# Optimization experiments

Measured on AMD Instinct MI355X. Metric: run time of the kernel, lower is better.

## Reference

```python
import jax, jax.numpy as jnp
import numpy as np
from jax import ops

NEG_SLOPE = 0.2
EPS = 1e-5


def layer_norm(v, g, b):
    mu = jnp.mean(v, axis=-1, keepdims=True)
    var = jnp.mean(jnp.square(v - mu), axis=-1, keepdims=True)
    return (v - mu) * jax.lax.rsqrt(var + EPS) * g + b


def gat_conv(x, src, dst, W, a_src, a_dst, bias, N, H, C, concat):
    # linear projection, per-head view [N, H, C]
    h = (x @ W).reshape(N, H, C)
    alpha_src = jnp.sum(h * a_src, axis=-1)  # [N, H]
    alpha_dst = jnp.sum(h * a_dst, axis=-1)  # [N, H]
    # per-edge raw attention logits [E, H]
    e = alpha_src[src] + alpha_dst[dst]
    e = jnp.where(e > 0, e, NEG_SLOPE * e)  # leaky relu
    # segment softmax over destination node
    m = ops.segment_max(e, dst, num_segments=N)  # [N, H]
    a = jnp.exp(e - m[dst])
    s = ops.segment_sum(a, dst, num_segments=N)  # [N, H]
    a = a / s[dst]
    # weighted scatter-aggregate: [E, H, C] messages -> [N, H, C]
    out = ops.segment_sum(h[src] * a[:, :, None], dst, num_segments=N)
    if concat:
        return out.reshape(N, H * C) + bias
    return jnp.mean(out, axis=1) + bias


def setup_inputs() -> dict:
    key = jax.random.key(0)
    ks = jax.random.split(key, 16)
    N, E, IN, H, C1, C2 = 50000, 800000, 128, 4, 64, 64
    sd_in = 1.0 / np.sqrt(IN)
    sd_h = 1.0 / np.sqrt(H * C1)
    return {
        "x": jax.random.normal(ks[0], (N, IN), jnp.float32),
        "edge_index": jax.random.randint(ks[1], (2, E), 0, N, jnp.int64),
        # GAT layer 1 (in -> H*C1, concat)
        "W1": jax.random.normal(ks[2], (IN, H * C1), jnp.float32) * sd_in,
        "att_src1": jax.random.normal(ks[3], (H, C1), jnp.float32) * sd_in,
        "att_dst1": jax.random.normal(ks[4], (H, C1), jnp.float32) * sd_in,
        "bias1": jnp.zeros((H * C1,), jnp.float32),
        "g1": jnp.ones((H * C1,), jnp.float32),
        "b1": jnp.zeros((H * C1,), jnp.float32),
        # GAT layer 2 (H*C1 -> C2, mean over heads)
        "W2": jax.random.normal(ks[5], (H * C1, H * C2), jnp.float32) * sd_h,
        "att_src2": jax.random.normal(ks[6], (H, C2), jnp.float32) * sd_h,
        "att_dst2": jax.random.normal(ks[7], (H, C2), jnp.float32) * sd_h,
        "bias2": jnp.zeros((C2,), jnp.float32),
        "g2": jnp.ones((C2,), jnp.float32),
        "b2": jnp.zeros((C2,), jnp.float32),
        # residual projection (in != out)
        "Wres": jax.random.normal(ks[8], (IN, C2), jnp.float32) * sd_in,
        "bres": jnp.zeros((C2,), jnp.float32),
    }


def reference(x, edge_index, W1, att_src1, att_dst1, bias1, g1, b1,
              W2, att_src2, att_dst2, bias2, g2, b2, Wres, bres):
    N = x.shape[0]
    H, C1 = att_src1.shape
    C2 = att_src2.shape[1]
    # PyG GATConv add_self_loops=True
    loop = jnp.arange(N, dtype=edge_index.dtype)
    src = jnp.concatenate([edge_index[0], loop])
    dst = jnp.concatenate([edge_index[1], loop])

    identity = x @ Wres + bres
    h1 = gat_conv(x, src, dst, W1, att_src1, att_dst1, bias1, N, H, C1, concat=True)
    h1 = jax.nn.elu(layer_norm(h1, g1, b1))  # dropout inactive (eval)
    h2 = gat_conv(h1, src, dst, W2, att_src2, att_dst2, bias2, N, H, C2, concat=False)
    h2 = layer_norm(h2, g2, b2)
    return jax.nn.elu(h2 + identity)
```

## Files before the change

### kernel.cpp

```cpp
#include <hip/hip_runtime.h>
#include <math.h>

#define HH 4
#define CC 64
#define HC 256
#define CAP 96

static constexpr float NEG_SLOPE = 0.2f;
static constexpr float LN_EPS = 1e-5f;

typedef __attribute__((ext_vector_type(8))) short short8;
typedef __attribute__((ext_vector_type(4))) float floatx4;
typedef __attribute__((ext_vector_type(4))) unsigned int uintx4;

__device__ __forceinline__ float bf2f(unsigned short u) {
  return __uint_as_float(((unsigned int)u) << 16);
}
__device__ __forceinline__ unsigned short f2bf(float f) {
  unsigned int u = __float_as_uint(f);
  u = (u + 0x7fff + ((u >> 16) & 1)) >> 16;
  return (unsigned short)u;
}
__device__ __forceinline__ unsigned int pack2bf(float a, float b) {
  return (unsigned int)f2bf(a) | ((unsigned int)f2bf(b) << 16);
}

__device__ __forceinline__ void macc8(float* acc, uintx4 h, float w) {
  acc[0] += w * __uint_as_float(h.x << 16);
  acc[1] += w * __uint_as_float(h.x & 0xffff0000u);
  acc[2] += w * __uint_as_float(h.y << 16);
  acc[3] += w * __uint_as_float(h.y & 0xffff0000u);
  acc[4] += w * __uint_as_float(h.z << 16);
  acc[5] += w * __uint_as_float(h.z & 0xffff0000u);
  acc[6] += w * __uint_as_float(h.w << 16);
  acc[7] += w * __uint_as_float(h.w & 0xffff0000u);
}

__device__ __forceinline__ short8 ldA8(const unsigned short* A, size_t idx) {
  return *(const short8*)(A + idx);
}
__device__ __forceinline__ short8 ldA8(const float* A, size_t idx) {
  const float4 u = *(const float4*)(A + idx);
  const float4 v = *(const float4*)(A + idx + 4);
  short8 r;
  r[0] = (short)f2bf(u.x); r[1] = (short)f2bf(u.y);
  r[2] = (short)f2bf(u.z); r[3] = (short)f2bf(u.w);
  r[4] = (short)f2bf(v.x); r[5] = (short)f2bf(v.y);
  r[6] = (short)f2bf(v.z); r[7] = (short)f2bf(v.w);
  return r;
}

__global__ __launch_bounds__(256) void prep_kernel(
    const float* __restrict__ W1, const float* __restrict__ W2,
    const float* __restrict__ Wres,
    unsigned short* __restrict__ wt1c, unsigned short* __restrict__ wt2,
    int* __restrict__ deg, int N) {
  const int idx = blockIdx.x * 256 + threadIdx.x;
  if (idx < 49152) {
    const int r = idx >> 7, k = idx & 127;
    float v = 0.f;
    if (r < 256) v = W1[k * 256 + r];
    else if (r < 320) v = Wres[k * 64 + (r - 256)];
    wt1c[idx] = f2bf(v);
  } else if (idx < 49152 + 65536) {
    const int i = idx - 49152;
    const int r = i >> 8, k = i & 255;
    wt2[i] = f2bf(W2[k * 256 + r]);
  } else if (idx < 49152 + 65536 + N) {
    deg[idx - 49152 - 65536] = 0;
  }
}

template <typename AT>
__global__ __launch_bounds__(256) void gemm128(
    const AT* __restrict__ A, const unsigned short* __restrict__ BT,
    unsigned short* __restrict__ Chm,
    float* __restrict__ ident, const float* __restrict__ bres,
    const float* __restrict__ att_src, const float* __restrict__ att_dst,
    float* __restrict__ as_, float* __restrict__ ad_,
    int M, int K, int GM,
    const int* __restrict__ srcs, const int* __restrict__ dsts,
    int* __restrict__ deg, int* __restrict__ col, int E, int N, int S) {
  const int bid = blockIdx.x;
  const int tid = threadIdx.x;
  int gid = bid;
  if (S > 0) {
    const int q = bid / 3;
    const bool is_scatter = (bid % 3 == 2) && (q < S);
    if (is_scatter) {
      const int base = q * 2048 + tid * 8;
#pragma unroll
      for (int k = 0; k < 8; ++k) {
        const int e = base + k;
        if (e < E + N) {
          int s, d;
          if (e < E) { s = srcs[e]; d = dsts[e]; }
          else       { s = e - E; d = s; }
          const int pos = atomicAdd(&deg[d], 1);
          col[d * CAP + pos] = s;
        }
      }
      return;
    }
    gid = bid - (q < S ? q : S);
  }
  const int bx = gid % GM, by = gid / GM;

  __shared__ unsigned short As[128][40];
  __shared__ unsigned short Bs[128][40];
  const int w = tid >> 6, lane = tid & 63;
  const int q4 = lane >> 4, mr = lane & 15;
  const int rh = w >> 1, ch = w & 1;
  const int row0 = bx * 128;
  const int col0 = by * 128;
  const int sr = tid >> 2;
  const int sk = (tid & 3) * 8;

  floatx4 acc[4][4] = {};

  short8 a0 = {}, a1 = {}, b0, b1;
  {
    const int r0 = row0 + sr, r1 = row0 + sr + 64;
    if (r0 < M) a0 = ldA8(A, (size_t)r0 * K + sk);
    if (r1 < M) a1 = ldA8(A, (size_t)r1 * K + sk);
    b0 = *(const short8*)(BT + (size_t)(col0 + sr) * K + sk);
    b1 = *(const short8*)(BT + (size_t)(col0 + sr + 64) * K + sk);
  }
  for (int k0 = 0; k0 < K; k0 += 32) {
    *(short8*)(&As[sr][sk]) = a0;
    *(short8*)(&As[sr + 64][sk]) = a1;
    *(short8*)(&Bs[sr][sk]) = b0;
    *(short8*)(&Bs[sr + 64][sk]) = b1;
    __syncthreads();
    const int kn = k0 + 32;
    if (kn < K) {
      const int r0 = row0 + sr, r1 = row0 + sr + 64;
      a0 = (r0 < M) ? ldA8(A, (size_t)r0 * K + kn + sk) : short8{};
      a1 = (r1 < M) ? ldA8(A, (size_t)r1 * K + kn + sk) : short8{};
      b0 = *(const short8*)(BT + (size_t)(col0 + sr) * K + kn + sk);
      b1 = *(const short8*)(BT + (size_t)(col0 + sr + 64) * K + kn + sk);
    }
    short8 af[4], bf[4];
#pragma unroll
    for (int i = 0; i < 4; ++i)
      af[i] = *(const short8*)(&As[rh * 64 + i * 16 + mr][q4 * 8]);
#pragma unroll
    for (int j = 0; j < 4; ++j)
      bf[j] = *(const short8*)(&Bs[ch * 64 + j * 16 + mr][q4 * 8]);
#pragma unroll
    for (int i = 0; i < 4; ++i)
#pragma unroll
      for (int j = 0; j < 4; ++j)
        acc[i][j] = __builtin_amdgcn_mfma_f32_16x16x32_bf16(af[i], bf[j], acc[i][j], 0, 0, 0);
    __syncthreads();
  }
  if (col0 < 256) {
    const int hh = (col0 >> 6) + ch;
#pragma unroll
    for (int i = 0; i < 4; ++i)
#pragma unroll
      for (int j = 0; j < 4; ++j)
#pragma unroll
        for (int rr = 0; rr < 4; ++rr) {
          const int row = row0 + rh * 64 + i * 16 + q4 * 4 + rr;
          if (row < M)
            Chm[((size_t)hh * M + row) * 64 + j * 16 + mr] = f2bf(acc[i][j][rr]);
        }
    float pa[16] = {}, pb[16] = {};
#pragma unroll
    for (int j = 0; j < 4; ++j) {
      const float a_s = att_src[hh * 64 + j * 16 + mr];
      const float a_d = att_dst[hh * 64 + j * 16 + mr];
#pragma unroll
      for (int i = 0; i < 4; ++i)
#pragma unroll
        for (int rr = 0; rr < 4; ++rr) {
          pa[i * 4 + rr] += acc[i][j][rr] * a_s;
          pb[i * 4 + rr] += acc[i][j][rr] * a_d;
        }
    }
#pragma unroll
    for (int off = 1; off < 16; off <<= 1) {
#pragma unroll
      for (int t = 0; t < 16; ++t) {
        pa[t] += __shfl_xor(pa[t], off);
        pb[t] += __shfl_xor(pb[t], off);
      }
    }
    if (mr == 0) {
#pragma unroll
      for (int i = 0; i < 4; ++i)
#pragma unroll
        for (int rr = 0; rr < 4; ++rr) {
          const int row = row0 + rh * 64 + i * 16 + q4 * 4 + rr;
          if (row < M) {
            as_[row * 4 + hh] = pa[i * 4 + rr];
            ad_[row * 4 + hh] = pb[i * 4 + rr];
          }
        }
    }
  } else if (ch == 0) {
#pragma unroll
    for (int i = 0; i < 4; ++i)
#pragma unroll
      for (int j = 0; j < 4; ++j)
#pragma unroll
        for (int rr = 0; rr < 4; ++rr) {
          const int row = row0 + rh * 64 + i * 16 + q4 * 4 + rr;
          if (row < M) {
            const int cc = j * 16 + mr;
            ident[(size_t)row * 64 + cc] = acc[i][j][rr] + bres[cc];
          }
        }
  }
}

__global__ __launch_bounds__(256) void agg_gather(
    const int* __restrict__ deg, const int* __restrict__ col,
    const float* __restrict__ as_, const float* __restrict__ ad_,
    const unsigned short* __restrict__ hlin_hm,
    unsigned short* __restrict__ agg, int N) {
  const int b = blockIdx.x;
  const int hh = b & 3;
  const int w = threadIdx.x >> 6, lane = threadIdx.x & 63;
  const int g = lane >> 4;
  const int sub = (lane >> 3) & 1;
  const int cg = lane & 7;
  const int el = lane & 15;
  const int gb = lane & 48;
  const int n = (b >> 3) * 32 + ((b >> 2) & 1) * 16 + w * 4 + g;
  const bool valid = n < N;
  const int n_c = valid ? n : 0;
  const uintx4* hb = (const uintx4*)(hlin_hm + (size_t)hh * N * 64) + cg;
  const float adv = ad_[n_c * 4 + hh];
  const int cnt = valid ? deg[n_c] : 0;
  const int* cbase = col + n_c * CAP;
  float acc[8] = {};
  float wsum = 0.f;
  for (int off = 0;; off += 16) {
    const int len = cnt - off;
    int lm = len > 16 ? 16 : (len < 0 ? 0 : len);
    lm = max(lm, __shfl_xor(lm, 16));
    lm = max(lm, __shfl_xor(lm, 32));
    if (lm == 0) break;
    int s_l = 0;
    float w_l = 0.f;
    if (el < len) {
      s_l = cbase[off + el];
      float v = as_[s_l * 4 + hh] + adv;
      v = v > 0.f ? v : NEG_SLOPE * v;
      w_l = __expf(v);
    }
    wsum += w_l;
    int j = 0;
    for (; j + 4 <= lm; j += 4) {
      const int sA = __shfl(s_l, gb + j + sub);
      const int sB = __shfl(s_l, gb + j + 2 + sub);
      const float wA = __shfl(w_l, gb + j + sub);
      const float wB = __shfl(w_l, gb + j + 2 + sub);
      const uintx4 hA = hb[(size_t)sA * 8];
      const uintx4 hB = hb[(size_t)sB * 8];
      macc8(acc, hA, wA);
      macc8(acc, hB, wB);
    }
    for (; j < lm; j += 2) {
      const int s = __shfl(s_l, gb + j + sub);
      const float wt = __shfl(w_l, gb + j + sub);
      macc8(acc, hb[(size_t)s * 8], wt);
    }
  }
  wsum += __shfl_xor(wsum, 1);
  wsum += __shfl_xor(wsum, 2);
  wsum += __shfl_xor(wsum, 4);
  wsum += __shfl_xor(wsum, 8);
#pragma unroll
  for (int t = 0; t < 8; ++t) acc[t] += __shfl_xor(acc[t], 8);
  if (sub == 0 && valid) {
    const float inv = 1.0f / wsum;
    uintx4 o;
    o.x = pack2bf(acc[0] * inv, acc[1] * inv);
    o.y = pack2bf(acc[2] * inv, acc[3] * inv);
    o.z = pack2bf(acc[4] * inv, acc[5] * inv);
    o.w = pack2bf(acc[6] * inv, acc[7] * inv);
    ((uintx4*)(agg + ((size_t)hh * N + n) * 64))[cg] = o;
  }
}

__global__ __launch_bounds__(256) void combine_ln1(
    const unsigned short* __restrict__ agg, const float* __restrict__ bias1,
    const float* __restrict__ g1, const float* __restrict__ b1,
    unsigned short* __restrict__ h1, int N) {
  const int n = blockIdx.x;
  const int tid = threadIdx.x;
  const int hh = tid >> 6, lane = tid & 63;
  const float val = bf2f(agg[((size_t)hh * N + n) * 64 + lane]) + bias1[tid];
  float s1 = val, s2 = val * val;
#pragma unroll
  for (int off = 32; off > 0; off >>= 1) {
    s1 += __shfl_down(s1, off);
    s2 += __shfl_down(s2, off);
  }
  __shared__ float ws1[4], ws2[4];
  if (lane == 0) { ws1[hh] = s1; ws2[hh] = s2; }
  __syncthreads();
  const float tot1 = ws1[0] + ws1[1] + ws1[2] + ws1[3];
  const float tot2 = ws2[0] + ws2[1] + ws2[2] + ws2[3];
  const float mu = tot1 * (1.0f / HC);
  const float var = tot2 * (1.0f / HC) - mu * mu;
  float y = (val - mu) * rsqrtf(var + LN_EPS) * g1[tid] + b1[tid];
  y = y > 0.f ? y : expm1f(y);
  h1[(size_t)n * HC + tid] = f2bf(y);
}

__global__ __launch_bounds__(256) void combine_final(
    const unsigned short* __restrict__ agg, const float* __restrict__ ident,
    const float* __restrict__ bias2, const float* __restrict__ g2,
    const float* __restrict__ b2, float* __restrict__ out, int N) {
  const int n = blockIdx.x * 4 + (threadIdx.x >> 6);
  const int c = threadIdx.x & 63;
  if (n >= N) return;
  float v = 0.25f * (bf2f(agg[((size_t)0 * N + n) * 64 + c]) +
                     bf2f(agg[((size_t)1 * N + n) * 64 + c]) +
                     bf2f(agg[((size_t)2 * N + n) * 64 + c]) +
                     bf2f(agg[((size_t)3 * N + n) * 64 + c])) +
            bias2[c];
  float s1 = v, s2 = v * v;
#pragma unroll
  for (int off = 32; off > 0; off >>= 1) {
    s1 += __shfl_down(s1, off);
    s2 += __shfl_down(s2, off);
  }
  s1 = __shfl(s1, 0);
  s2 = __shfl(s2, 0);
  const float mu = s1 * (1.0f / 64.0f);
  const float var = s2 * (1.0f / 64.0f) - mu * mu;
  float y = (v - mu) * rsqrtf(var + LN_EPS) * g2[c] + b2[c];
  y += ident[(size_t)n * 64 + c];
  out[(size_t)n * 64 + c] = y > 0.f ? y : expm1f(y);
}

extern "C" void kernel_launch(void* const* d_in, const int* in_sizes, int n_in,
                              void* d_out, int out_size, void* d_ws, size_t ws_size,
                              hipStream_t stream) {
  const float* x        = (const float*)d_in[0];
  const int*   ei       = (const int*)d_in[1];
  const float* W1       = (const float*)d_in[2];
  const float* att_src1 = (const float*)d_in[3];
  const float* att_dst1 = (const float*)d_in[4];
  const float* bias1    = (const float*)d_in[5];
  const float* g1       = (const float*)d_in[6];
  const float* b1       = (const float*)d_in[7];
  const float* W2       = (const float*)d_in[8];
  const float* att_src2 = (const float*)d_in[9];
  const float* att_dst2 = (const float*)d_in[10];
  const float* bias2    = (const float*)d_in[11];
  const float* g2       = (const float*)d_in[12];
  const float* b2       = (const float*)d_in[13];
  const float* Wres     = (const float*)d_in[14];
  const float* bres     = (const float*)d_in[15];

  const int N = in_sizes[0] / 128;
  const int E = in_sizes[1] / 2;
  const int IN = 128;

  const int* srcs = ei;
  const int* dsts = ei + E;

  char* p = (char*)d_ws;
  auto alloc = [&](size_t bytes) {
    char* r = p;
    p += (bytes + 255) & ~(size_t)255;
    return r;
  };
  float* ident  = (float*)alloc((size_t)N * 64 * 4);
  float* as_    = (float*)alloc((size_t)N * HH * 4);
  float* ad_    = (float*)alloc((size_t)N * HH * 4);
  int* deg      = (int*)alloc((size_t)N * 4);
  int* col      = (int*)alloc((size_t)N * CAP * 4);
  unsigned short* hlin_hm = (unsigned short*)alloc((size_t)N * HC * 2);
  unsigned short* h1b     = (unsigned short*)alloc((size_t)N * HC * 2);
  unsigned short* aggb    = (unsigned short*)alloc((size_t)4 * N * 64 * 2);
  unsigned short* wt1c = (unsigned short*)alloc((size_t)384 * IN * 2);
  unsigned short* wt2  = (unsigned short*)alloc((size_t)HC * HC * 2);

  const int m128 = (N + 127) / 128;
  const int prep_items = 49152 + 65536 + N;
  const int gatherblocks = ((N + 31) / 32) * 8;
  const int G1 = m128 * 3;
  const int S  = (E + N + 2047) / 2048;
  dim3 blk(256);

  prep_kernel<<<(prep_items + 255) / 256, blk, 0, stream>>>(
      W1, W2, Wres, wt1c, wt2, deg, N);

  gemm128<float><<<G1 + S, blk, 0, stream>>>(
      x, wt1c, hlin_hm, ident, bres, att_src1, att_dst1, as_, ad_, N, IN, m128,
      srcs, dsts, deg, col, E, N, S);
  agg_gather<<<gatherblocks, blk, 0, stream>>>(deg, col, as_, ad_, hlin_hm, aggb, N);
  combine_ln1<<<N, blk, 0, stream>>>(aggb, bias1, g1, b1, h1b, N);

  gemm128<unsigned short><<<m128 * 2, blk, 0, stream>>>(
      h1b, wt2, hlin_hm, nullptr, nullptr, att_src2, att_dst2, as_, ad_, N, HC, m128,
      nullptr, nullptr, nullptr, nullptr, 0, N, 0);
  agg_gather<<<gatherblocks, blk, 0, stream>>>(deg, col, as_, ad_, hlin_hm, aggb, N);
  combine_final<<<(N + 3) / 4, blk, 0, stream>>>(aggb, ident, bias2, g2, b2,
                                                 (float*)d_out, N);
}
```

Baseline: 335.4 us.

## Use a full-width 128x256 tile GEMM for layer 2 and coarsen edge scatter

Adds a 512-thread gemm256 kernel for the layer-2 projection. Each block computes all 256 output columns (every head) for a 128-row tile, so each A tile is loaded once instead of twice across two column-half blocks. The fused attention-logit reductions stay in the new kernel. Separately, each scatter block in the layer-1 GEMM launch now handles 4096 edges instead of 2048, halving the number of interleaved scatter blocks. In exchange, the new GEMM uses more shared memory and threads per block and launches fewer blocks, which may lower occupancy and load balance.

```diff
diff --git a/kernel.cpp b/kernel.cpp
--- a/kernel.cpp
+++ b/kernel.cpp
@@ -88,9 +88,9 @@
     const int q = bid / 3;
     const bool is_scatter = (bid % 3 == 2) && (q < S);
     if (is_scatter) {
-      const int base = q * 2048 + tid * 8;
-#pragma unroll
-      for (int k = 0; k < 8; ++k) {
+      const int base = q * 4096 + tid * 16;
+#pragma unroll
+      for (int k = 0; k < 16; ++k) {
         const int e = base + k;
         if (e < E + N) {
           int s, d;
@@ -212,6 +212,101 @@
             ident[(size_t)row * 64 + cc] = acc[i][j][rr] + bres[cc];
           }
         }
+  }
+}
+
+__global__ __launch_bounds__(512) void gemm256(
+    const unsigned short* __restrict__ A, const unsigned short* __restrict__ BT,
+    unsigned short* __restrict__ Chm,
+    const float* __restrict__ att_src, const float* __restrict__ att_dst,
+    float* __restrict__ as_, float* __restrict__ ad_, int M, int K) {
+  __shared__ unsigned short As[128][40];
+  __shared__ unsigned short Bs[256][40];
+  const int tid = threadIdx.x;
+  const int w = tid >> 6, lane = tid & 63;
+  const int q4 = lane >> 4, mr = lane & 15;
+  const int rh = w >> 2, ch = w & 3;
+  const int row0 = blockIdx.x * 128;
+  const int sr = tid >> 2;
+  const int sk = (tid & 3) * 8;
+
+  floatx4 acc[4][4] = {};
+  short8 a0 = {}, b0, b1;
+  {
+    const int r0 = row0 + sr;
+    if (r0 < M) a0 = ldA8(A, (size_t)r0 * K + sk);
+    b0 = *(const short8*)(BT + (size_t)sr * K + sk);
+    b1 = *(const short8*)(BT + (size_t)(sr + 128) * K + sk);
+  }
+  for (int k0 = 0; k0 < K; k0 += 32) {
+    *(short8*)(&As[sr][sk]) = a0;
+    *(short8*)(&Bs[sr][sk]) = b0;
+    *(short8*)(&Bs[sr + 128][sk]) = b1;
+    __syncthreads();
+    const int kn = k0 + 32;
+    if (kn < K) {
+      const int r0 = row0 + sr;
+      a0 = (r0 < M) ? ldA8(A, (size_t)r0 * K + kn + sk) : short8{};
+      b0 = *(const short8*)(BT + (size_t)sr * K + kn + sk);
+      b1 = *(const short8*)(BT + (size_t)(sr + 128) * K + kn + sk);
+    }
+    short8 af[4], bf[4];
+#pragma unroll
+    for (int i = 0; i < 4; ++i)
+      af[i] = *(const short8*)(&As[rh * 64 + i * 16 + mr][q4 * 8]);
+#pragma unroll
+    for (int j = 0; j < 4; ++j)
+      bf[j] = *(const short8*)(&Bs[ch * 64 + j * 16 + mr][q4 * 8]);
+#pragma unroll
+    for (int i = 0; i < 4; ++i)
+#pragma unroll
+      for (int j = 0; j < 4; ++j)
+        acc[i][j] = __builtin_amdgcn_mfma_f32_16x16x32_bf16(af[i], bf[j], acc[i][j], 0, 0, 0);
+    __syncthreads();
+  }
+  const int hh = ch;
+#pragma unroll
+  for (int i = 0; i < 4; ++i)
+#pragma unroll
+    for (int j = 0; j < 4; ++j)
+#pragma unroll
+      for (int rr = 0; rr < 4; ++rr) {
+        const int row = row0 + rh * 64 + i * 16 + q4 * 4 + rr;
+        if (row < M)
+          Chm[((size_t)hh * M + row) * 64 + j * 16 + mr] = f2bf(acc[i][j][rr]);
+      }
+  float pa[16] = {}, pb[16] = {};
+#pragma unroll
+  for (int j = 0; j < 4; ++j) {
+    const float a_s = att_src[hh * 64 + j * 16 + mr];
+    const float a_d = att_dst[hh * 64 + j * 16 + mr];
+#pragma unroll
+    for (int i = 0; i < 4; ++i)
+#pragma unroll
+      for (int rr = 0; rr < 4; ++rr) {
+        pa[i * 4 + rr] += acc[i][j][rr] * a_s;
+        pb[i * 4 + rr] += acc[i][j][rr] * a_d;
+      }
+  }
+#pragma unroll
+  for (int off = 1; off < 16; off <<= 1) {
+#pragma unroll
+    for (int t = 0; t < 16; ++t) {
+      pa[t] += __shfl_xor(pa[t], off);
+      pb[t] += __shfl_xor(pb[t], off);
+    }
+  }
+  if (mr == 0) {
+#pragma unroll
+    for (int i = 0; i < 4; ++i)
+#pragma unroll
+      for (int rr = 0; rr < 4; ++rr) {
+        const int row = row0 + rh * 64 + i * 16 + q4 * 4 + rr;
+        if (row < M) {
+          as_[row * 4 + hh] = pa[i * 4 + rr];
+          ad_[row * 4 + hh] = pb[i * 4 + rr];
+        }
+      }
   }
 }
 
@@ -387,7 +482,7 @@
   const int prep_items = 49152 + 65536 + N;
   const int gatherblocks = ((N + 31) / 32) * 8;
   const int G1 = m128 * 3;
-  const int S  = (E + N + 2047) / 2048;
+  const int S  = (E + N + 4095) / 4096;
   dim3 blk(256);
 
   prep_kernel<<<(prep_items + 255) / 256, blk, 0, stream>>>(
@@ -399,9 +494,8 @@
   agg_gather<<<gatherblocks, blk, 0, stream>>>(deg, col, as_, ad_, hlin_hm, aggb, N);
   combine_ln1<<<N, blk, 0, stream>>>(aggb, bias1, g1, b1, h1b, N);
 
-  gemm128<unsigned short><<<m128 * 2, blk, 0, stream>>>(
-      h1b, wt2, hlin_hm, nullptr, nullptr, att_src2, att_dst2, as_, ad_, N, HC, m128,
-      nullptr, nullptr, nullptr, nullptr, 0, N, 0);
+  gemm256<<<m128, dim3(512), 0, stream>>>(
+      h1b, wt2, hlin_hm, att_src2, att_dst2, as_, ad_, N, HC);
   agg_gather<<<gatherblocks, blk, 0, stream>>>(deg, col, as_, ad_, hlin_hm, aggb, N);
   combine_final<<<(N + 3) / 4, blk, 0, stream>>>(aggb, ident, bias2, g2, b2,
                                                  (float*)d_out, N);
```

Measured after the change: 329.3 us. About the same (-1.8%).
